# Kernel optimization log

Hardware: AMD Instinct MI355X
Metric: run time of the kernel (lower is better)

Reference implementation:

```python
import jax, jax.numpy as jnp
import numpy as np

D_MODEL = 1024
N_HEAD = 16
HEAD_DIM = D_MODEL // N_HEAD
D_FF = 4096
N_EXPERTS = 4
EPS = 1e-05


def _layer_norm(x, gamma, beta):
    mu = jnp.mean(x, axis=-1, keepdims=True)
    var = jnp.mean((x - mu) ** 2, axis=-1, keepdims=True)
    return (x - mu) / jnp.sqrt(var + EPS) * gamma + beta


def setup_inputs() -> dict:
    key = jax.random.key(0)
    ks = jax.random.split(key, 20)
    f32 = jnp.float32
    sc = 1.0 / np.sqrt(D_MODEL)
    scf = 1.0 / np.sqrt(D_FF)
    return {
        "src": jax.random.normal(ks[0], (4, 512, D_MODEL), f32),
        "Wq": jax.random.normal(ks[1], (D_MODEL, D_MODEL), f32) * sc,
        "bq": jnp.zeros((D_MODEL,), f32),
        "Wk": jax.random.normal(ks[2], (D_MODEL, D_MODEL), f32) * sc,
        "bk": jnp.zeros((D_MODEL,), f32),
        "Wv": jax.random.normal(ks[3], (D_MODEL, D_MODEL), f32) * sc,
        "bv": jnp.zeros((D_MODEL,), f32),
        "Wo": jax.random.normal(ks[4], (D_MODEL, D_MODEL), f32) * sc,
        "bo": jnp.zeros((D_MODEL,), f32),
        "router_w": jax.random.normal(ks[5], (D_MODEL, 1), f32) * 0.05,
        "router_b": jnp.zeros((1,), f32),
        "W1": jax.random.normal(ks[6], (N_EXPERTS, D_MODEL, D_FF), f32) * sc,
        "b1": jnp.zeros((N_EXPERTS, D_FF), f32),
        "W2": jax.random.normal(ks[7], (N_EXPERTS, D_FF, D_MODEL), f32) * scf,
        "b2": jnp.zeros((N_EXPERTS, D_MODEL), f32),
        "ln1_g": jnp.ones((D_MODEL,), f32),
        "ln1_b": jnp.zeros((D_MODEL,), f32),
        "ln2_g": jnp.ones((D_MODEL,), f32),
        "ln2_b": jnp.zeros((D_MODEL,), f32),
    }


def reference(src, Wq, bq, Wk, bk, Wv, bv, Wo, bo, router_w, router_b,
              W1, b1, W2, b2, ln1_g, ln1_b, ln2_g, ln2_b):
    B, T, _ = src.shape
    # --- self attention ---
    q = (src @ Wq + bq).reshape(B, T, N_HEAD, HEAD_DIM)
    k = (src @ Wk + bk).reshape(B, T, N_HEAD, HEAD_DIM)
    v = (src @ Wv + bv).reshape(B, T, N_HEAD, HEAD_DIM)
    scale = HEAD_DIM ** -0.5
    scores = jnp.einsum('bqhd,bkhd->bhqk', q, k) * scale
    probs = jax.nn.softmax(scores, axis=-1)
    attn = jnp.einsum('bhqk,bkhd->bqhd', probs, v).reshape(B, T, D_MODEL)
    attn = attn @ Wo + bo
    x = _layer_norm(src + attn, ln1_g, ln1_b)
    # --- hash-routed single-expert MoE FFN ---
    keys = (x @ router_w + router_b)[..., 0]           # [B, T]
    expert_idx = jnp.remainder(jnp.floor(keys).astype(jnp.int32), N_EXPERTS)
    ff_out = jnp.zeros_like(x)
    for e in range(N_EXPERTS):
        h = jax.nn.relu(x @ W1[e] + b1[e])             # [B, T, D_FF]
        y = h @ W2[e] + b2[e]                          # [B, T, D_MODEL]
        ff_out = ff_out + jnp.where((expert_idx == e)[..., None], y, 0.0)
    return _layer_norm(x + ff_out, ln2_g, ln2_b)
```

## Files before the change

kernel.cpp:

```cpp
#include <hip/hip_runtime.h>
#include <hip/hip_bf16.h>
#include <stdint.h>

typedef unsigned short u16;
typedef __attribute__((ext_vector_type(8))) short s8v;
typedef __attribute__((ext_vector_type(4))) float f4v;

#define DEVI static __device__ __forceinline__

DEVI u16 f2bf(float x) {
  union { float f; unsigned u; } a; a.f = x;
  return (u16)((a.u + 0x7fffu + ((a.u >> 16) & 1u)) >> 16);
}
DEVI float bf2f(u16 h) {
  union { float f; unsigned u; } a; a.u = ((unsigned)h) << 16; return a.f;
}
DEVI float wred_add(float s) {
#pragma unroll
  for (int o = 32; o; o >>= 1) s += __shfl_xor(s, o, 64);
  return s;
}
DEVI float wred_max(float s) {
#pragma unroll
  for (int o = 32; o; o >>= 1) s = fmaxf(s, __shfl_xor(s, o, 64));
  return s;
}
DEVI f4v mfma16(s8v a, s8v b, f4v c) {
  return __builtin_amdgcn_mfma_f32_16x16x32_bf16(a, b, c, 0, 0, 0);
}

DEVI int rho(int j) { return ((j & 12) << 1) | (j & 3) | ((j >> 4) << 2); }

DEVI void gload16(const u16* gp, u16* lp) {
  __builtin_amdgcn_global_load_lds(
      (const __attribute__((address_space(1))) uint32_t*)gp,
      (__attribute__((address_space(3))) uint32_t*)lp, 16, 0, 0);
}

DEVI s8v ldfrag_sw(const u16* base, int r, int lg) {
  int off = ((r >> 4) << 9) + ((r & 15) << 5) + ((lg ^ ((r >> 1) & 3)) << 3);
  return *(const s8v*)(base + off);
}

__global__ __launch_bounds__(256) void split_k(const float* __restrict__ in,
                                               u16* __restrict__ h, u16* __restrict__ l, int n4) {
  int i = blockIdx.x * 256 + threadIdx.x;
  if (i >= n4) return;
  float4 v = ((const float4*)in)[i];
  ushort4 hv, lv;
  hv.x = f2bf(v.x); lv.x = f2bf(v.x - bf2f(hv.x));
  hv.y = f2bf(v.y); lv.y = f2bf(v.y - bf2f(hv.y));
  hv.z = f2bf(v.z); lv.z = f2bf(v.z - bf2f(hv.z));
  hv.w = f2bf(v.w); lv.w = f2bf(v.w - bf2f(hv.w));
  int t = i & 7, blk = i >> 3;
  int si = blk * 8 + ((t & 3) << 1) + (t >> 2);
  ((ushort4*)h)[si] = hv;
  ((ushort4*)l)[si] = lv;
}

template<bool LO>
__global__ __launch_bounds__(256) void transpose_split_k(const float* __restrict__ in, long long zIn,
                                                         u16* __restrict__ outH, u16* __restrict__ outL,
                                                         long long zOut, int R, int C) {
  __shared__ float t[32][33];
  in += (long long)blockIdx.z * zIn;
  outH += (long long)blockIdx.z * zOut;
  if (LO) outL += (long long)blockIdx.z * zOut;
  const int cc = blockIdx.x * 32, rr = blockIdx.y * 32;
  const int tx = threadIdx.x, ty = threadIdx.y;
#pragma unroll
  for (int i = 0; i < 4; ++i)
    t[ty * 4 + i][tx] = in[(long long)(rr + ty * 4 + i) * C + cc + tx];
  __syncthreads();
  const int rtx = rho(tx);
#pragma unroll
  for (int i = 0; i < 4; ++i) {
    float v = t[tx][ty * 4 + i];
    long long o = (long long)(cc + ty * 4 + i) * R + rr + rtx;
    u16 h = f2bf(v);
    outH[o] = h;
    if (LO) outL[o] = f2bf(v - bf2f(h));
  }
}

__global__ __launch_bounds__(256) void transpose_pair_k(const u16* __restrict__ inH, const u16* __restrict__ inL,
                                                        u16* __restrict__ oH, u16* __restrict__ oL) {
  __shared__ u16 th[32][34], tl[32][34];
  const int b = blockIdx.z;
  const int dd = blockIdx.x * 32;
  const int tt = blockIdx.y * 32;
  const int tx = threadIdx.x, ty = threadIdx.y;
  const int64_t ibase = ((int64_t)(b * 512 + tt)) * 3072 + 2048 + dd;
  const int rtx = rho(tx);
#pragma unroll
  for (int i = 0; i < 4; ++i) {
    int rr = ty * 4 + i;
    th[rr][tx] = inH[ibase + (int64_t)rr * 3072 + rtx];
    tl[rr][tx] = inL[ibase + (int64_t)rr * 3072 + rtx];
  }
  __syncthreads();
  const int64_t obase = ((int64_t)b * 1024 + dd) * 512 + tt;
#pragma unroll
  for (int i = 0; i < 4; ++i) {
    int rr = ty * 4 + i;
    oH[obase + (int64_t)rr * 512 + rtx] = th[tx][rr];
    oL[obase + (int64_t)rr * 512 + rtx] = tl[tx][rr];
  }
}

__global__ __launch_bounds__(256) void catb_k(const float* __restrict__ a, const float* __restrict__ b,
                                              const float* __restrict__ c, float* __restrict__ o) {
  int i = blockIdx.x * 256 + threadIdx.x;
  if (i >= 3072) return;
  o[i] = i < 1024 ? a[i] : (i < 2048 ? b[i - 1024] : c[i - 2048]);
}

struct GemmArgs {
  const u16* Ah; const u16* Al; int lda;
  const u16* Bh; const u16* Bl; int ldb;
  float* C; u16* Ch; u16* Cl; int ldc;
  const float* bias;
  int K;
  int Z2;
  int64_t aZ1, aZ2, bZ1, bZ2, cZ1, cZ2;
  const int* ofs;
  int64_t bStrE; int biasStrE;
};

template<int BM, int BN, bool SPLIT, int EPI, bool PN>
__global__ __launch_bounds__(256, 3) void gemm_k(GemmArgs g) {
  constexpr int ASZ = BM * 32, BSZ = BN * 32;
  constexpr int AN = SPLIT ? 2 * ASZ : ASZ;
  constexpr int BNT = SPLIT ? 2 * BSZ : BSZ;
  constexpr int NLOAD = (BM / 64 + BN / 64) * (SPLIT ? 2 : 1);
  __shared__ __align__(16) u16 sA[2][AN];
  __shared__ __align__(16) u16 sB[2][BNT];

  const int tid = threadIdx.x;
  const u16* Ah = g.Ah; const u16* Al = g.Al;
  const u16* Bh = g.Bh; const u16* Bl = g.Bl;
  int64_t cOff = 0;
  if (g.Z2 > 0) {
    int z1 = blockIdx.z / g.Z2, z2 = blockIdx.z % g.Z2;
    int64_t ao = (int64_t)z1 * g.aZ1 + (int64_t)z2 * g.aZ2;
    int64_t bo = (int64_t)z1 * g.bZ1 + (int64_t)z2 * g.bZ2;
    Ah += ao; Bh += bo;
    if (SPLIT) { Al += ao; Bl += bo; }
    cOff = (int64_t)z1 * g.cZ1 + (int64_t)z2 * g.cZ2;
  }
  const int row0 = blockIdx.x * BM;
  const int col0 = blockIdx.y * BN;
  const float* bias = g.bias;
  if (g.ofs) {
    if (row0 >= g.ofs[4]) return;
    int e = 0;
    while (e < 3 && row0 >= g.ofs[e + 1]) ++e;
    Bh += (int64_t)e * g.bStrE;
    if (bias) bias += (int64_t)e * g.biasStrE;
  }

  const int w = tid >> 6, lane = tid & 63;
  const int wr = w >> 1, wc = w & 1;
  const int lr = lane & 15, lg = lane >> 4;
  constexpr int FM = BM / 32, FN = BN / 32;

  const int srow = lane >> 2;
  const int sG = (lane & 3) ^ ((lane >> 3) & 3);

  auto stage = [&](int b, int kt) {
#pragma unroll
    for (int c = 0; c < BM / 64; ++c) {
      int ch = c * 4 + w;
      int64_t go = (int64_t)(row0 + ch * 16 + srow) * g.lda + kt + sG * 8;
      gload16(Ah + go, &sA[b][ch * 512]);
      if (SPLIT) gload16(Al + go, &sA[b][ASZ + ch * 512]);
    }
#pragma unroll
    for (int c = 0; c < BN / 64; ++c) {
      int ch = c * 4 + w;
      int64_t go = (int64_t)(col0 + ch * 16 + srow) * g.ldb + kt + sG * 8;
      gload16(Bh + go, &sB[b][ch * 512]);
      if (SPLIT) gload16(Bl + go, &sB[b][BSZ + ch * 512]);
    }
  };

  f4v acc[FM][FN];
#pragma unroll
  for (int i = 0; i < FM; ++i)
#pragma unroll
    for (int j = 0; j < FN; ++j) acc[i][j] = f4v{0.f, 0.f, 0.f, 0.f};

  s8v a0[FM], b0[FN], al0[SPLIT ? FM : 1], bl0[SPLIT ? FN : 1];
  s8v a1[FM], b1[FN], al1[SPLIT ? FM : 1], bl1[SPLIT ? FN : 1];

  auto rdfrags = [&](int buf, auto& af, auto& bf, auto& afl, auto& bfl) {
#pragma unroll
    for (int mi = 0; mi < FM; ++mi) {
      int r = wr * (BM / 2) + mi * 16 + lr;
      af[mi] = ldfrag_sw(&sA[buf][0], r, lg);
      if (SPLIT) afl[mi] = ldfrag_sw(&sA[buf][ASZ], r, lg);
    }
#pragma unroll
    for (int ni = 0; ni < FN; ++ni) {
      int r = wc * (BN / 2) + ni * 16 + lr;
      bf[ni] = ldfrag_sw(&sB[buf][0], r, lg);
      if (SPLIT) bfl[ni] = ldfrag_sw(&sB[buf][BSZ], r, lg);
    }
  };

  const int nt = g.K >> 5;

  stage(0, 0);
  stage(1, 32);
  asm volatile("s_waitcnt vmcnt(%0)" :: "n"(NLOAD) : "memory");
  __builtin_amdgcn_sched_barrier(0);
  __builtin_amdgcn_s_barrier();
  rdfrags(0, a0, b0, al0, bl0);

  auto body = [&](int t, auto& cA, auto& cB, auto& cAl, auto& cBl,
                  auto& nA, auto& nB, auto& nAl, auto& nBl) {
    asm volatile("s_waitcnt lgkmcnt(0)" ::: "memory");
    __builtin_amdgcn_sched_barrier(0);
    __builtin_amdgcn_s_barrier();
    if (t + 2 < nt) stage(t & 1, (t + 2) << 5);
    if (t + 1 < nt) {
      if (t + 2 < nt)
        asm volatile("s_waitcnt vmcnt(%0)" :: "n"(NLOAD) : "memory");
      else
        asm volatile("s_waitcnt vmcnt(0)" ::: "memory");
      __builtin_amdgcn_sched_barrier(0);
      __builtin_amdgcn_s_barrier();
      rdfrags((t + 1) & 1, nA, nB, nAl, nBl);
    }
    __builtin_amdgcn_s_setprio(1);
#pragma unroll
    for (int mi = 0; mi < FM; ++mi)
#pragma unroll
      for (int ni = 0; ni < FN; ++ni) {
        acc[mi][ni] = mfma16(cA[mi], cB[ni], acc[mi][ni]);
        if (SPLIT) {
          acc[mi][ni] = mfma16(cA[mi], cBl[ni], acc[mi][ni]);
          acc[mi][ni] = mfma16(cAl[mi], cB[ni], acc[mi][ni]);
        }
      }
    __builtin_amdgcn_s_setprio(0);
  };

  for (int t = 0; t < nt; t += 2) {
    body(t,     a0, b0, al0, bl0, a1, b1, al1, bl1);
    body(t + 1, a1, b1, al1, bl1, a0, b0, al0, bl0);
  }

#pragma unroll
  for (int mi = 0; mi < FM; ++mi) {
    int rbase = row0 + wr * (BM / 2) + mi * 16 + lg * 4;
#pragma unroll
    for (int ni = 0; ni < FN; ++ni) {
      int c = col0 + wc * (BN / 2) + ni * 16 + lr;
      int cs = c;
      if (PN) {
        int jr = ((lr >> 2) << 3) | (lr & 3) | ((ni & 1) << 2);
        cs = (c & ~31) | jr;
      }
      float bv = bias ? bias[c] : 0.f;
#pragma unroll
      for (int j = 0; j < 4; ++j) {
        int r = rbase + j;
        float v = acc[mi][ni][j] + bv;
        if (EPI == 0) {
          g.C[cOff + (int64_t)r * g.ldc + cs] = v;
        } else if (EPI == 1) {
          u16 h = f2bf(v);
          int64_t o = cOff + (int64_t)r * g.ldc + cs;
          g.Ch[o] = h;
          g.Cl[o] = f2bf(v - bf2f(h));
        } else {
          v = v > 0.f ? v : 0.f;
          g.Ch[cOff + (int64_t)r * g.ldc + cs] = f2bf(v);
        }
      }
    }
  }
}

__global__ __launch_bounds__(256) void reduce_k(const float* __restrict__ part, const int* __restrict__ rowsrc,
                                                const int* __restrict__ ofs, const float* __restrict__ b2,
                                                float* __restrict__ y) {
  int r = blockIdx.x;
  if (r >= ofs[4]) return;
  int s = rowsrc[r];
  if (s < 0) return;
  int e = 0;
  while (e < 3 && r >= ofs[e + 1]) ++e;
  int c = threadIdx.x;
  const int64_t RN = 2560ll * 1024;
  float4 v0 = ((const float4*)(part + 0 * RN + (int64_t)r * 1024))[c];
  float4 v1 = ((const float4*)(part + 1 * RN + (int64_t)r * 1024))[c];
  float4 bb = ((const float4*)(b2 + (int64_t)e * 1024))[c];
  float4 o;
  o.x = (v0.x + v1.x) + bb.x;
  o.y = (v0.y + v1.y) + bb.y;
  o.z = (v0.z + v1.z) + bb.z;
  o.w = (v0.w + v1.w) + bb.w;
  ((float4*)(y + (int64_t)s * 1024))[c] = o;
}

__global__ __launch_bounds__(128) void softmax_k(float* __restrict__ scores) {
  __shared__ float sm[2];
  const int64_t row = blockIdx.x;
  float* p = scores + row * 512;
  const int tid = threadIdx.x, w = tid >> 6, lane = tid & 63;
  float4 v = ((const float4*)p)[tid];
  v.x *= 0.125f; v.y *= 0.125f; v.z *= 0.125f; v.w *= 0.125f;
  float m = wred_max(fmaxf(fmaxf(v.x, v.y), fmaxf(v.z, v.w)));
  if (lane == 0) sm[w] = m;
  __syncthreads();
  m = fmaxf(sm[0], sm[1]);
  float e0 = expf(v.x - m), e1 = expf(v.y - m), e2 = expf(v.z - m), e3 = expf(v.w - m);
  float s = wred_add(e0 + e1 + e2 + e3);
  __syncthreads();
  if (lane == 0) sm[w] = s;
  __syncthreads();
  float inv = 1.f / (sm[0] + sm[1]);
  e0 *= inv; e1 *= inv; e2 *= inv; e3 *= inv;
  u16* ph = (u16*)p;
  ushort4 hv, lv;
  hv.x = f2bf(e0); lv.x = f2bf(e0 - bf2f(hv.x));
  hv.y = f2bf(e1); lv.y = f2bf(e1 - bf2f(hv.y));
  hv.z = f2bf(e2); lv.z = f2bf(e2 - bf2f(hv.z));
  hv.w = f2bf(e3); lv.w = f2bf(e3 - bf2f(hv.w));
  ((ushort4*)ph)[tid] = hv;
  ((ushort4*)(ph + 512))[tid] = lv;
}

__global__ __launch_bounds__(256) void ln_k(const float* __restrict__ a, const float* __restrict__ b,
                                            const float* __restrict__ gm, const float* __restrict__ bt,
                                            float* __restrict__ out) {
  __shared__ float sm[4];
  const int r = blockIdx.x, tid = threadIdx.x;
  const int w = tid >> 6, lane = tid & 63;
  float4 va = ((const float4*)(a + (int64_t)r * 1024))[tid];
  float4 vb = ((const float4*)(b + (int64_t)r * 1024))[tid];
  float x0 = va.x + vb.x, x1 = va.y + vb.y, x2 = va.z + vb.z, x3 = va.w + vb.w;
  float s = wred_add(x0 + x1 + x2 + x3);
  if (lane == 0) sm[w] = s;
  __syncthreads();
  float mu = (sm[0] + sm[1] + sm[2] + sm[3]) * (1.f / 1024.f);
  float d0 = x0 - mu, d1 = x1 - mu, d2 = x2 - mu, d3 = x3 - mu;
  float q = wred_add(d0 * d0 + d1 * d1 + d2 * d2 + d3 * d3);
  __syncthreads();
  if (lane == 0) sm[w] = q;
  __syncthreads();
  float var = (sm[0] + sm[1] + sm[2] + sm[3]) * (1.f / 1024.f);
  float rs = 1.f / sqrtf(var + 1e-5f);
  float4 g4 = ((const float4*)gm)[tid];
  float4 b4 = ((const float4*)bt)[tid];
  float4 o;
  o.x = d0 * rs * g4.x + b4.x;
  o.y = d1 * rs * g4.y + b4.y;
  o.z = d2 * rs * g4.z + b4.z;
  o.w = d3 * rs * g4.w + b4.w;
  ((float4*)(out + (int64_t)r * 1024))[tid] = o;
}

__global__ __launch_bounds__(256) void router_k(const float* __restrict__ x, const float* __restrict__ rw,
                                                const float* __restrict__ rb, int* __restrict__ eidx) {
  int t = blockIdx.x * 4 + (threadIdx.x >> 6);
  int lane = threadIdx.x & 63;
  const float* xr = x + (int64_t)t * 1024;
  float s = 0.f;
#pragma unroll
  for (int i = 0; i < 16; ++i) {
    int c = i * 64 + lane;
    s += xr[c] * rw[c];
  }
  s = wred_add(s);
  if (lane == 0) {
    float key = s + rb[0];
    int f = (int)floorf(key);
    eidx[t] = f & 3;
  }
}

__global__ __launch_bounds__(256) void compact_k(const int* __restrict__ eidx,
                                                 int* __restrict__ rowsrc, int* __restrict__ ofs) {
  __shared__ unsigned long long sc[256];
  __shared__ int soff[5];
  const int tid = threadIdx.x;
  int myE[8];
  unsigned long long c = 0;
#pragma unroll
  for (int i = 0; i < 8; ++i) {
    int e = eidx[tid * 8 + i];
    myE[i] = e;
    c += 1ull << (e * 16);
  }
  sc[tid] = c;
  __syncthreads();
  for (int o = 1; o < 256; o <<= 1) {
    unsigned long long v = (tid >= o) ? sc[tid - o] : 0ull;
    __syncthreads();
    sc[tid] += v;
    __syncthreads();
  }
  unsigned long long incl = sc[tid], tot = sc[255];
  unsigned long long excl = incl - c;
  if (tid == 0) {
    int off = 0;
    for (int e = 0; e < 4; ++e) {
      soff[e] = off;
      int cnt = (int)((tot >> (e * 16)) & 0xffff);
      off += (cnt + 127) & ~127;
    }
    soff[4] = off;
    for (int e = 0; e < 5; ++e) ofs[e] = soff[e];
  }
  __syncthreads();
  for (int r = tid; r < 2560; r += 256) rowsrc[r] = -1;
  __threadfence_block();
  __syncthreads();
  int rank[4];
#pragma unroll
  for (int e = 0; e < 4; ++e) rank[e] = (int)((excl >> (e * 16)) & 0xffff);
#pragma unroll
  for (int i = 0; i < 8; ++i) {
    int e = myE[i];
    rowsrc[soff[e] + rank[e]] = tid * 8 + i;
    rank[e]++;
  }
}

__global__ __launch_bounds__(256) void gather_k(const float* __restrict__ x, const int* __restrict__ rowsrc,
                                                const int* __restrict__ ofs, u16* __restrict__ xg) {
  int r = blockIdx.x;
  if (r >= ofs[4]) return;
  int s = rowsrc[r];
  int c = threadIdx.x;
  float4 v = (s >= 0) ? ((const float4*)(x + (int64_t)s * 1024))[c] : float4{0.f, 0.f, 0.f, 0.f};
  ushort4 o;
  o.x = f2bf(v.x); o.y = f2bf(v.y); o.z = f2bf(v.z); o.w = f2bf(v.w);
  int t = c & 7, blk = c >> 3;
  int si = blk * 8 + ((t & 3) << 1) + (t >> 2);
  ((ushort4*)(xg + (int64_t)r * 1024))[si] = o;
}

extern "C" void kernel_launch(void* const* d_in, const int* in_sizes, int n_in,
                              void* d_out, int out_size, void* d_ws, size_t ws_size,
                              hipStream_t stream) {
  const float* src = (const float*)d_in[0];
  const float* Wq  = (const float*)d_in[1];
  const float* bq  = (const float*)d_in[2];
  const float* Wk  = (const float*)d_in[3];
  const float* bk  = (const float*)d_in[4];
  const float* Wv  = (const float*)d_in[5];
  const float* bv  = (const float*)d_in[6];
  const float* Wo  = (const float*)d_in[7];
  const float* bo  = (const float*)d_in[8];
  const float* rw  = (const float*)d_in[9];
  const float* rb  = (const float*)d_in[10];
  const float* W1  = (const float*)d_in[11];
  const float* b1  = (const float*)d_in[12];
  const float* W2  = (const float*)d_in[13];
  const float* b2  = (const float*)d_in[14];
  const float* g1  = (const float*)d_in[15];
  const float* be1 = (const float*)d_in[16];
  const float* g2  = (const float*)d_in[17];
  const float* be2 = (const float*)d_in[18];
  float* out = (float*)d_out;

  char* base = (char*)d_ws;
  size_t off = 0;
  auto alloc = [&](size_t bytes) -> char* {
    char* p = base + off;
    off += (bytes + 255) & ~(size_t)255;
    return p;
  };
  const size_t MB = 1ull << 20;
  u16* srcH = (u16*)alloc(4 * MB);
  u16* srcL = (u16*)alloc(4 * MB);
  u16* WqkvTh = (u16*)alloc(6 * MB);
  u16* WqkvTl = (u16*)alloc(6 * MB);
  u16* WoTh = (u16*)alloc(2 * MB);
  u16* WoTl = (u16*)alloc(2 * MB);
  float* bqkv = (float*)alloc(16 * 1024);
  u16* qkvH = (u16*)alloc(12 * MB);
  u16* qkvL = (u16*)alloc(12 * MB);
  u16* hbuf = (u16*)qkvH;
  u16* vTH = (u16*)alloc(4 * MB); u16* vTL = (u16*)alloc(4 * MB);
  float* scores = (float*)alloc(64 * MB);
  u16* W1T = (u16*)scores;
  u16* W2T = (u16*)scores + 16ull * 1024 * 1024;
  u16* attnH = (u16*)alloc(4 * MB); u16* attnL = (u16*)alloc(4 * MB);
  u16* xg = (u16*)attnH;
  float* woOut = (float*)alloc(8 * MB);
  float* ybuf = (float*)woOut;
  float* xbuf = (float*)alloc(8 * MB);
  float* partials = (float*)alloc(20 * MB);
  int* eidx   = (int*)alloc(2048 * 4);
  int* rowsrc = (int*)alloc(2560 * 4);
  int* ofs    = (int*)alloc(32);
  (void)ws_size; (void)in_sizes; (void)n_in; (void)out_size;

  dim3 tb(32, 8);

  split_k<<<2048, 256, 0, stream>>>(src, srcH, srcL, 2048 * 1024 / 4);
  transpose_split_k<true><<<dim3(32, 32, 1), tb, 0, stream>>>(Wq, 0, WqkvTh, WqkvTl, 0, 1024, 1024);
  transpose_split_k<true><<<dim3(32, 32, 1), tb, 0, stream>>>(Wk, 0, WqkvTh + 1024 * 1024, WqkvTl + 1024 * 1024, 0, 1024, 1024);
  transpose_split_k<true><<<dim3(32, 32, 1), tb, 0, stream>>>(Wv, 0, WqkvTh + 2 * 1024 * 1024, WqkvTl + 2 * 1024 * 1024, 0, 1024, 1024);
  transpose_split_k<true><<<dim3(32, 32, 1), tb, 0, stream>>>(Wo, 0, WoTh, WoTl, 0, 1024, 1024);
  catb_k<<<12, 256, 0, stream>>>(bq, bk, bv, bqkv);

  {
    GemmArgs g{};
    g.Ah = srcH; g.Al = srcL; g.lda = 1024;
    g.Bh = WqkvTh; g.Bl = WqkvTl; g.ldb = 1024;
    g.Ch = qkvH; g.Cl = qkvL; g.ldc = 3072;
    g.bias = bqkv; g.K = 1024; g.Z2 = 0;
    gemm_k<128, 64, true, 1, true><<<dim3(16, 48, 1), 256, 0, stream>>>(g);
  }
  transpose_pair_k<<<dim3(32, 16, 4), tb, 0, stream>>>(qkvH, qkvL, vTH, vTL);

  {
    GemmArgs g{};
    g.Ah = qkvH; g.Al = qkvL; g.lda = 3072;
    g.Bh = qkvH + 1024; g.Bl = qkvL + 1024; g.ldb = 3072;
    g.C = scores; g.ldc = 512;
    g.K = 64; g.Z2 = 16;
    g.aZ1 = 512ll * 3072; g.aZ2 = 64;
    g.bZ1 = 512ll * 3072; g.bZ2 = 64;
    g.cZ1 = 16ll * 512 * 512; g.cZ2 = 512ll * 512;
    gemm_k<128, 64, true, 0, true><<<dim3(4, 8, 64), 256, 0, stream>>>(g);
  }
  softmax_k<<<64 * 512, 128, 0, stream>>>(scores);
  {
    GemmArgs g{};
    g.Ah = (const u16*)scores; g.Al = (const u16*)scores + 512; g.lda = 1024;
    g.Bh = vTH; g.Bl = vTL; g.ldb = 512;
    g.Ch = attnH; g.Cl = attnL; g.ldc = 1024;
    g.K = 512; g.Z2 = 16;
    g.aZ1 = 16ll * 512 * 1024; g.aZ2 = 512ll * 1024;
    g.bZ1 = 1024ll * 512;      g.bZ2 = 64ll * 512;
    g.cZ1 = 512ll * 1024;      g.cZ2 = 64;
    gemm_k<64, 64, true, 1, true><<<dim3(8, 1, 64), 256, 0, stream>>>(g);
  }
  {
    GemmArgs g{};
    g.Ah = attnH; g.Al = attnL; g.lda = 1024;
    g.Bh = WoTh; g.Bl = WoTl; g.ldb = 1024;
    g.C = woOut; g.ldc = 1024;
    g.bias = bo; g.K = 1024; g.Z2 = 0;
    gemm_k<64, 64, true, 0, false><<<dim3(32, 16, 1), 256, 0, stream>>>(g);
  }
  ln_k<<<2048, 256, 0, stream>>>(src, woOut, g1, be1, xbuf);

  router_k<<<512, 256, 0, stream>>>(xbuf, rw, rb, eidx);
  compact_k<<<1, 256, 0, stream>>>(eidx, rowsrc, ofs);
  gather_k<<<2560, 256, 0, stream>>>(xbuf, rowsrc, ofs, xg);

  transpose_split_k<false><<<dim3(128, 32, 4), tb, 0, stream>>>(W1, 1024ll * 4096, W1T, nullptr, 4096ll * 1024, 1024, 4096);
  transpose_split_k<false><<<dim3(32, 128, 4), tb, 0, stream>>>(W2, 4096ll * 1024, W2T, nullptr, 1024ll * 4096, 4096, 1024);

  {
    GemmArgs g{};
    g.Ah = xg; g.lda = 1024;
    g.Bh = W1T; g.ldb = 1024;
    g.Ch = hbuf; g.ldc = 4096;
    g.bias = b1; g.biasStrE = 4096;
    g.K = 1024; g.Z2 = 0;
    g.ofs = ofs; g.bStrE = 4096ll * 1024;
    gemm_k<128, 128, false, 2, true><<<dim3(20, 32, 1), 256, 0, stream>>>(g);
  }
  {
    GemmArgs g{};
    g.Ah = hbuf; g.lda = 4096;
    g.Bh = W2T; g.ldb = 4096;
    g.C = partials; g.ldc = 1024;
    g.bias = nullptr;
    g.K = 2048; g.Z2 = 2;
    g.aZ1 = 0; g.aZ2 = 2048;
    g.bZ1 = 0; g.bZ2 = 2048;
    g.cZ1 = 0; g.cZ2 = 2560ll * 1024;
    g.ofs = ofs; g.bStrE = 4096ll * 1024;
    gemm_k<128, 64, false, 0, false><<<dim3(20, 16, 2), 256, 0, stream>>>(g);
  }
  reduce_k<<<2560, 256, 0, stream>>>(partials, rowsrc, ofs, b2, ybuf);
  ln_k<<<2048, 256, 0, stream>>>(xbuf, ybuf, g2, be2, out);
}
```

Before: 316.4 us.

## Vectorize weight transposes, widen QKV tile, fuse LN with router and reduce

The weight transpose kernel now processes 32x128 tiles with float4 loads and ushort4 stores instead of scalar element accesses. The QKV GEMM moves to a 128x96 tile with a min-waves launch bound of 2, and the GEMM load staging is generalized to handle non-64-multiple tiles. LayerNorm1 is fused with the router dot product, and the expert partial-sum reduce is fused with the final LayerNorm, which removes two kernel launches and one round trip through memory. The cost is a larger shared-memory tile in the transpose, lower occupancy for the QKV GEMM, and an added block-wide reduction in the LN kernel.

Result: faster. 310.1 us (-2.0%).

```diff
diff --git a/kernel.cpp b/kernel.cpp
--- a/kernel.cpp
+++ b/kernel.cpp
@@ -62,24 +62,36 @@
 __global__ __launch_bounds__(256) void transpose_split_k(const float* __restrict__ in, long long zIn,
                                                          u16* __restrict__ outH, u16* __restrict__ outL,
                                                          long long zOut, int R, int C) {
-  __shared__ float t[32][33];
+  __shared__ float t[32][132];
   in += (long long)blockIdx.z * zIn;
   outH += (long long)blockIdx.z * zOut;
   if (LO) outL += (long long)blockIdx.z * zOut;
-  const int cc = blockIdx.x * 32, rr = blockIdx.y * 32;
-  const int tx = threadIdx.x, ty = threadIdx.y;
-#pragma unroll
-  for (int i = 0; i < 4; ++i)
-    t[ty * 4 + i][tx] = in[(long long)(rr + ty * 4 + i) * C + cc + tx];
-  __syncthreads();
-  const int rtx = rho(tx);
+  const int cc = blockIdx.x * 128, rr = blockIdx.y * 32;
+  const int id = threadIdx.y * 32 + threadIdx.x;
 #pragma unroll
   for (int i = 0; i < 4; ++i) {
-    float v = t[tx][ty * 4 + i];
-    long long o = (long long)(cc + ty * 4 + i) * R + rr + rtx;
-    u16 h = f2bf(v);
-    outH[o] = h;
-    if (LO) outL[o] = f2bf(v - bf2f(h));
+    int slot = i * 256 + id;
+    int r = slot >> 5, c4 = slot & 31;
+    float4 v = *(const float4*)&in[(long long)(rr + r) * C + cc + c4 * 4];
+    *(float4*)&t[r][c4 * 4] = v;
+  }
+  __syncthreads();
+#pragma unroll
+  for (int i = 0; i < 4; ++i) {
+    int slot = i * 256 + id;
+    int j = slot >> 3, gs = slot & 7;
+    int r0 = gs * 4;
+    float v0 = t[r0 + 0][j], v1 = t[r0 + 1][j], v2 = t[r0 + 2][j], v3 = t[r0 + 3][j];
+    long long o = (long long)(cc + j) * R + rr + 8 * (gs & 3) + 4 * (gs >> 2);
+    ushort4 hv;
+    hv.x = f2bf(v0); hv.y = f2bf(v1); hv.z = f2bf(v2); hv.w = f2bf(v3);
+    *(ushort4*)&outH[o] = hv;
+    if (LO) {
+      ushort4 lv;
+      lv.x = f2bf(v0 - bf2f(hv.x)); lv.y = f2bf(v1 - bf2f(hv.y));
+      lv.z = f2bf(v2 - bf2f(hv.z)); lv.w = f2bf(v3 - bf2f(hv.w));
+      *(ushort4*)&outL[o] = lv;
+    }
   }
 }
 
@@ -127,12 +139,16 @@
   int64_t bStrE; int biasStrE;
 };
 
-template<int BM, int BN, bool SPLIT, int EPI, bool PN>
-__global__ __launch_bounds__(256, 3) void gemm_k(GemmArgs g) {
+template<int BM, int BN, bool SPLIT, int EPI, bool PN, int MINW>
+__global__ __launch_bounds__(256, MINW) void gemm_k(GemmArgs g) {
   constexpr int ASZ = BM * 32, BSZ = BN * 32;
   constexpr int AN = SPLIT ? 2 * ASZ : ASZ;
   constexpr int BNT = SPLIT ? 2 * BSZ : BSZ;
-  constexpr int NLOAD = (BM / 64 + BN / 64) * (SPLIT ? 2 : 1);
+  constexpr int nA = BM / 16, nB = BN / 16;
+  constexpr int nAt = SPLIT ? 2 * nA : nA;
+  constexpr int TOT = nAt + (SPLIT ? 2 * nB : nB);
+  static_assert(TOT % 4 == 0, "chunk count must divide across 4 waves");
+  constexpr int NLOAD = TOT / 4;
   __shared__ __align__(16) u16 sA[2][AN];
   __shared__ __align__(16) u16 sB[2][BNT];
 
@@ -169,18 +185,24 @@
 
   auto stage = [&](int b, int kt) {
 #pragma unroll
-    for (int c = 0; c < BM / 64; ++c) {
-      int ch = c * 4 + w;
-      int64_t go = (int64_t)(row0 + ch * 16 + srow) * g.lda + kt + sG * 8;
-      gload16(Ah + go, &sA[b][ch * 512]);
-      if (SPLIT) gload16(Al + go, &sA[b][ASZ + ch * 512]);
-    }
-#pragma unroll
-    for (int c = 0; c < BN / 64; ++c) {
-      int ch = c * 4 + w;
-      int64_t go = (int64_t)(col0 + ch * 16 + srow) * g.ldb + kt + sG * 8;
-      gload16(Bh + go, &sB[b][ch * 512]);
-      if (SPLIT) gload16(Bl + go, &sB[b][BSZ + ch * 512]);
+    for (int c = 0; c < NLOAD; ++c) {
+      int s = c * 4 + w;
+      if (s < nA) {
+        int64_t go = (int64_t)(row0 + s * 16 + srow) * g.lda + kt + sG * 8;
+        gload16(Ah + go, &sA[b][s * 512]);
+      } else if (SPLIT && s < 2 * nA) {
+        int ch = s - nA;
+        int64_t go = (int64_t)(row0 + ch * 16 + srow) * g.lda + kt + sG * 8;
+        gload16(Al + go, &sA[b][ASZ + ch * 512]);
+      } else if (s < nAt + nB) {
+        int ch = s - nAt;
+        int64_t go = (int64_t)(col0 + ch * 16 + srow) * g.ldb + kt + sG * 8;
+        gload16(Bh + go, &sB[b][ch * 512]);
+      } else {
+        int ch = s - nAt - nB;
+        int64_t go = (int64_t)(col0 + ch * 16 + srow) * g.ldb + kt + sG * 8;
+        gload16(Bl + go, &sB[b][BSZ + ch * 512]);
+      }
     }
   };
 
@@ -218,7 +240,7 @@
   rdfrags(0, a0, b0, al0, bl0);
 
   auto body = [&](int t, auto& cA, auto& cB, auto& cAl, auto& cBl,
-                  auto& nA, auto& nB, auto& nAl, auto& nBl) {
+                  auto& nA_, auto& nB_, auto& nAl_, auto& nBl_) {
     asm volatile("s_waitcnt lgkmcnt(0)" ::: "memory");
     __builtin_amdgcn_sched_barrier(0);
     __builtin_amdgcn_s_barrier();
@@ -230,8 +252,9 @@
         asm volatile("s_waitcnt vmcnt(0)" ::: "memory");
       __builtin_amdgcn_sched_barrier(0);
       __builtin_amdgcn_s_barrier();
-      rdfrags((t + 1) & 1, nA, nB, nAl, nBl);
+      rdfrags((t + 1) & 1, nA_, nB_, nAl_, nBl_);
     }
+    __builtin_amdgcn_sched_barrier(0);
     __builtin_amdgcn_s_setprio(1);
 #pragma unroll
     for (int mi = 0; mi < FM; ++mi)
@@ -257,11 +280,7 @@
 #pragma unroll
     for (int ni = 0; ni < FN; ++ni) {
       int c = col0 + wc * (BN / 2) + ni * 16 + lr;
-      int cs = c;
-      if (PN) {
-        int jr = ((lr >> 2) << 3) | (lr & 3) | ((ni & 1) << 2);
-        cs = (c & ~31) | jr;
-      }
+      int cs = PN ? ((c & ~31) | rho(c & 31)) : c;
       float bv = bias ? bias[c] : 0.f;
 #pragma unroll
       for (int j = 0; j < 4; ++j) {
@@ -283,28 +302,6 @@
   }
 }
 
-__global__ __launch_bounds__(256) void reduce_k(const float* __restrict__ part, const int* __restrict__ rowsrc,
-                                                const int* __restrict__ ofs, const float* __restrict__ b2,
-                                                float* __restrict__ y) {
-  int r = blockIdx.x;
-  if (r >= ofs[4]) return;
-  int s = rowsrc[r];
-  if (s < 0) return;
-  int e = 0;
-  while (e < 3 && r >= ofs[e + 1]) ++e;
-  int c = threadIdx.x;
-  const int64_t RN = 2560ll * 1024;
-  float4 v0 = ((const float4*)(part + 0 * RN + (int64_t)r * 1024))[c];
-  float4 v1 = ((const float4*)(part + 1 * RN + (int64_t)r * 1024))[c];
-  float4 bb = ((const float4*)(b2 + (int64_t)e * 1024))[c];
-  float4 o;
-  o.x = (v0.x + v1.x) + bb.x;
-  o.y = (v0.y + v1.y) + bb.y;
-  o.z = (v0.z + v1.z) + bb.z;
-  o.w = (v0.w + v1.w) + bb.w;
-  ((float4*)(y + (int64_t)s * 1024))[c] = o;
-}
-
 __global__ __launch_bounds__(128) void softmax_k(float* __restrict__ scores) {
   __shared__ float sm[2];
   const int64_t row = blockIdx.x;
@@ -333,9 +330,10 @@
   ((ushort4*)(ph + 512))[tid] = lv;
 }
 
-__global__ __launch_bounds__(256) void ln_k(const float* __restrict__ a, const float* __restrict__ b,
-                                            const float* __restrict__ gm, const float* __restrict__ bt,
-                                            float* __restrict__ out) {
+__global__ __launch_bounds__(256) void ln_router_k(const float* __restrict__ a, const float* __restrict__ b,
+                                                   const float* __restrict__ gm, const float* __restrict__ bt,
+                                                   const float* __restrict__ rw, const float* __restrict__ rb,
+                                                   float* __restrict__ out, int* __restrict__ eidx) {
   __shared__ float sm[4];
   const int r = blockIdx.x, tid = threadIdx.x;
   const int w = tid >> 6, lane = tid & 63;
@@ -361,25 +359,57 @@
   o.z = d2 * rs * g4.z + b4.z;
   o.w = d3 * rs * g4.w + b4.w;
   ((float4*)(out + (int64_t)r * 1024))[tid] = o;
-}
-
-__global__ __launch_bounds__(256) void router_k(const float* __restrict__ x, const float* __restrict__ rw,
-                                                const float* __restrict__ rb, int* __restrict__ eidx) {
-  int t = blockIdx.x * 4 + (threadIdx.x >> 6);
-  int lane = threadIdx.x & 63;
-  const float* xr = x + (int64_t)t * 1024;
-  float s = 0.f;
-#pragma unroll
-  for (int i = 0; i < 16; ++i) {
-    int c = i * 64 + lane;
-    s += xr[c] * rw[c];
-  }
-  s = wred_add(s);
-  if (lane == 0) {
-    float key = s + rb[0];
-    int f = (int)floorf(key);
-    eidx[t] = f & 3;
-  }
+  float4 w4 = ((const float4*)rw)[tid];
+  float p = o.x * w4.x + o.y * w4.y + o.z * w4.z + o.w * w4.w;
+  p = wred_add(p);
+  __syncthreads();
+  if (lane == 0) sm[w] = p;
+  __syncthreads();
+  if (tid == 0) {
+    float key = (sm[0] + sm[1] + sm[2] + sm[3]) + rb[0];
+    eidx[r] = (int)floorf(key) & 3;
+  }
+}
+
+__global__ __launch_bounds__(256) void reduce_ln_k(const float* __restrict__ part, const int* __restrict__ rowsrc,
+                                                   const int* __restrict__ ofs, const float* __restrict__ b2,
+                                                   const float* __restrict__ xb, const float* __restrict__ gm,
+                                                   const float* __restrict__ bt, float* __restrict__ out) {
+  __shared__ float sm[4];
+  const int r = blockIdx.x;
+  if (r >= ofs[4]) return;
+  const int s = rowsrc[r];
+  if (s < 0) return;
+  int e = 0;
+  while (e < 3 && r >= ofs[e + 1]) ++e;
+  const int tid = threadIdx.x, w = tid >> 6, lane = tid & 63;
+  const int64_t RN = 2560ll * 1024;
+  float4 v0 = ((const float4*)(part + 0 * RN + (int64_t)r * 1024))[tid];
+  float4 v1 = ((const float4*)(part + 1 * RN + (int64_t)r * 1024))[tid];
+  float4 bb = ((const float4*)(b2 + (int64_t)e * 1024))[tid];
+  float4 va = ((const float4*)(xb + (int64_t)s * 1024))[tid];
+  float y0 = (v0.x + v1.x) + bb.x, y1 = (v0.y + v1.y) + bb.y;
+  float y2 = (v0.z + v1.z) + bb.z, y3 = (v0.w + v1.w) + bb.w;
+  float x0 = va.x + y0, x1 = va.y + y1, x2 = va.z + y2, x3 = va.w + y3;
+  float sum = wred_add(x0 + x1 + x2 + x3);
+  if (lane == 0) sm[w] = sum;
+  __syncthreads();
+  float mu = (sm[0] + sm[1] + sm[2] + sm[3]) * (1.f / 1024.f);
+  float d0 = x0 - mu, d1 = x1 - mu, d2 = x2 - mu, d3 = x3 - mu;
+  float q = wred_add(d0 * d0 + d1 * d1 + d2 * d2 + d3 * d3);
+  __syncthreads();
+  if (lane == 0) sm[w] = q;
+  __syncthreads();
+  float var = (sm[0] + sm[1] + sm[2] + sm[3]) * (1.f / 1024.f);
+  float rs = 1.f / sqrtf(var + 1e-5f);
+  float4 g4 = ((const float4*)gm)[tid];
+  float4 b4 = ((const float4*)bt)[tid];
+  float4 o;
+  o.x = d0 * rs * g4.x + b4.x;
+  o.y = d1 * rs * g4.y + b4.y;
+  o.z = d2 * rs * g4.z + b4.z;
+  o.w = d3 * rs * g4.w + b4.w;
+  ((float4*)(out + (int64_t)s * 1024))[tid] = o;
 }
 
 __global__ __launch_bounds__(256) void compact_k(const int* __restrict__ eidx,
@@ -493,7 +523,6 @@
   u16* attnH = (u16*)alloc(4 * MB); u16* attnL = (u16*)alloc(4 * MB);
   u16* xg = (u16*)attnH;
   float* woOut = (float*)alloc(8 * MB);
-  float* ybuf = (float*)woOut;
   float* xbuf = (float*)alloc(8 * MB);
   float* partials = (float*)alloc(20 * MB);
   int* eidx   = (int*)alloc(2048 * 4);
@@ -504,10 +533,10 @@
   dim3 tb(32, 8);
 
   split_k<<<2048, 256, 0, stream>>>(src, srcH, srcL, 2048 * 1024 / 4);
-  transpose_split_k<true><<<dim3(32, 32, 1), tb, 0, stream>>>(Wq, 0, WqkvTh, WqkvTl, 0, 1024, 1024);
-  transpose_split_k<true><<<dim3(32, 32, 1), tb, 0, stream>>>(Wk, 0, WqkvTh + 1024 * 1024, WqkvTl + 1024 * 1024, 0, 1024, 1024);
-  transpose_split_k<true><<<dim3(32, 32, 1), tb, 0, stream>>>(Wv, 0, WqkvTh + 2 * 1024 * 1024, WqkvTl + 2 * 1024 * 1024, 0, 1024, 1024);
-  transpose_split_k<true><<<dim3(32, 32, 1), tb, 0, stream>>>(Wo, 0, WoTh, WoTl, 0, 1024, 1024);
+  transpose_split_k<true><<<dim3(8, 32, 1), tb, 0, stream>>>(Wq, 0, WqkvTh, WqkvTl, 0, 1024, 1024);
+  transpose_split_k<true><<<dim3(8, 32, 1), tb, 0, stream>>>(Wk, 0, WqkvTh + 1024 * 1024, WqkvTl + 1024 * 1024, 0, 1024, 1024);
+  transpose_split_k<true><<<dim3(8, 32, 1), tb, 0, stream>>>(Wv, 0, WqkvTh + 2 * 1024 * 1024, WqkvTl + 2 * 1024 * 1024, 0, 1024, 1024);
+  transpose_split_k<true><<<dim3(8, 32, 1), tb, 0, stream>>>(Wo, 0, WoTh, WoTl, 0, 1024, 1024);
   catb_k<<<12, 256, 0, stream>>>(bq, bk, bv, bqkv);
 
   {
@@ -516,7 +545,7 @@
     g.Bh = WqkvTh; g.Bl = WqkvTl; g.ldb = 1024;
     g.Ch = qkvH; g.Cl = qkvL; g.ldc = 3072;
     g.bias = bqkv; g.K = 1024; g.Z2 = 0;
-    gemm_k<128, 64, true, 1, true><<<dim3(16, 48, 1), 256, 0, stream>>>(g);
+    gemm_k<128, 96, true, 1, true, 2><<<dim3(16, 32, 1), 256, 0, stream>>>(g);
   }
   transpose_pair_k<<<dim3(32, 16, 4), tb, 0, stream>>>(qkvH, qkvL, vTH, vTL);
 
@@ -529,7 +558,7 @@
     g.aZ1 = 512ll * 3072; g.aZ2 = 64;
     g.bZ1 = 512ll * 3072; g.bZ2 = 64;
     g.cZ1 = 16ll * 512 * 512; g.cZ2 = 512ll * 512;
-    gemm_k<128, 64, true, 0, true><<<dim3(4, 8, 64), 256, 0, stream>>>(g);
+    gemm_k<128, 64, true, 0, true, 3><<<dim3(4, 8, 64), 256, 0, stream>>>(g);
   }
   softmax_k<<<64 * 512, 128, 0, stream>>>(scores);
   {
@@ -541,7 +570,7 @@
     g.aZ1 = 16ll * 512 * 1024; g.aZ2 = 512ll * 1024;
     g.bZ1 = 1024ll * 512;      g.bZ2 = 64ll * 512;
     g.cZ1 = 512ll * 1024;      g.cZ2 = 64;
-    gemm_k<64, 64, true, 1, true><<<dim3(8, 1, 64), 256, 0, stream>>>(g);
+    gemm_k<64, 64, true, 1, true, 3><<<dim3(8, 1, 64), 256, 0, stream>>>(g);
   }
   {
     GemmArgs g{};
@@ -549,16 +578,15 @@
     g.Bh = WoTh; g.Bl = WoTl; g.ldb = 1024;
     g.C = woOut; g.ldc = 1024;
     g.bias = bo; g.K = 1024; g.Z2 = 0;
-    gemm_k<64, 64, true, 0, false><<<dim3(32, 16, 1), 256, 0, stream>>>(g);
-  }
-  ln_k<<<2048, 256, 0, stream>>>(src, woOut, g1, be1, xbuf);
-
-  router_k<<<512, 256, 0, stream>>>(xbuf, rw, rb, eidx);
+    gemm_k<64, 64, true, 0, false, 3><<<dim3(32, 16, 1), 256, 0, stream>>>(g);
+  }
+  ln_router_k<<<2048, 256, 0, stream>>>(src, woOut, g1, be1, rw, rb, xbuf, eidx);
+
   compact_k<<<1, 256, 0, stream>>>(eidx, rowsrc, ofs);
   gather_k<<<2560, 256, 0, stream>>>(xbuf, rowsrc, ofs, xg);
 
-  transpose_split_k<false><<<dim3(128, 32, 4), tb, 0, stream>>>(W1, 1024ll * 4096, W1T, nullptr, 4096ll * 1024, 1024, 4096);
-  transpose_split_k<false><<<dim3(32, 128, 4), tb, 0, stream>>>(W2, 4096ll * 1024, W2T, nullptr, 1024ll * 4096, 4096, 1024);
+  transpose_split_k<false><<<dim3(32, 32, 4), tb, 0, stream>>>(W1, 1024ll * 4096, W1T, nullptr, 4096ll * 1024, 1024, 4096);
+  transpose_split_k<false><<<dim3(8, 128, 4), tb, 0, stream>>>(W2, 4096ll * 1024, W2T, nullptr, 1024ll * 4096, 4096, 1024);
 
   {
     GemmArgs g{};
@@ -568,7 +596,7 @@
     g.bias = b1; g.biasStrE = 4096;
     g.K = 1024; g.Z2 = 0;
     g.ofs = ofs; g.bStrE = 4096ll * 1024;
-    gemm_k<128, 128, false, 2, true><<<dim3(20, 32, 1), 256, 0, stream>>>(g);
+    gemm_k<128, 128, false, 2, true, 3><<<dim3(20, 32, 1), 256, 0, stream>>>(g);
   }
   {
     GemmArgs g{};
@@ -581,8 +609,7 @@
     g.bZ1 = 0; g.bZ2 = 2048;
     g.cZ1 = 0; g.cZ2 = 2560ll * 1024;
     g.ofs = ofs; g.bStrE = 4096ll * 1024;
-    gemm_k<128, 64, false, 0, false><<<dim3(20, 16, 2), 256, 0, stream>>>(g);
-  }
-  reduce_k<<<2560, 256, 0, stream>>>(partials, rowsrc, ofs, b2, ybuf);
-  ln_k<<<2048, 256, 0, stream>>>(xbuf, ybuf, g2, be2, out);
-}
+    gemm_k<128, 64, false, 0, false, 3><<<dim3(20, 16, 2), 256, 0, stream>>>(g);
+  }
+  reduce_ln_k<<<2560, 256, 0, stream>>>(partials, rowsrc, ofs, b2, xbuf, g2, be2, out);
+}
```
